# Optimization experiments

Measured on AMD Instinct MI355X. Metric: run time of the kernel, lower is better.

## Reference

```python
import jax, jax.numpy as jnp
import numpy as np

N, E, B = 30000, 240000, 64
F, H, T = 64, 4, 3
BOT = 256


def _gat_layer(x, e_src, e_dst, lin_w, att_src, att_dst, bias):
    # x: [N, in]; lin_w: [in, H*F]; att_*: [H, F]; bias: [H*F]
    xs = (x @ lin_w).reshape(N, H, F)                     # [N,H,F]
    a_src = jnp.einsum('nhf,hf->nh', xs, att_src)         # [N,H]
    a_dst = jnp.einsum('nhf,hf->nh', xs, att_dst)
    logits = jax.nn.leaky_relu(a_src[e_src] + a_dst[e_dst], negative_slope=0.2)  # [E2,H]
    m = jax.ops.segment_max(logits, e_dst, num_segments=N)        # softmax over in-edges per dst
    ex = jnp.exp(logits - m[e_dst])
    denom = jax.ops.segment_sum(ex, e_dst, num_segments=N)
    alpha = ex / (denom[e_dst] + 1e-16)                   # [E2,H]
    msg = alpha[:, :, None] * xs[e_src]                   # [E2,H,F]
    out = jax.ops.segment_sum(msg, e_dst, num_segments=N).reshape(N, H * F)
    return out + bias


def setup_inputs() -> dict:
    key = jax.random.key(0)
    ks = jax.random.split(key, 20)
    s = 0.1
    inp = {
        'street_feature': jax.random.normal(ks[0], (N, 5), jnp.float32),
        'edge_index': jax.random.randint(ks[1], (2, E), 0, N, dtype=jnp.int64),
        'batch': jnp.sort(jax.random.randint(ks[2], (N,), 0, B, dtype=jnp.int64)),
        'bbox_w': jax.random.normal(ks[3], (5, F), jnp.float32) * s,
        'bbox_b': jnp.zeros((F,), jnp.float32),
        'lin_w0': jax.random.normal(ks[4], (F, H * F), jnp.float32) * s,
        'att_src0': jax.random.normal(ks[5], (H, F), jnp.float32) * s,
        'att_dst0': jax.random.normal(ks[6], (H, F), jnp.float32) * s,
        'bias0': jnp.zeros((H * F,), jnp.float32),
        'lin_w1': jax.random.normal(ks[7], (H * F, H * F), jnp.float32) * s,
        'att_src1': jax.random.normal(ks[8], (H, F), jnp.float32) * s,
        'att_dst1': jax.random.normal(ks[9], (H, F), jnp.float32) * s,
        'bias1': jnp.zeros((H * F,), jnp.float32),
        'lin_w2': jax.random.normal(ks[10], (H * F, H * F), jnp.float32) * s,
        'att_src2': jax.random.normal(ks[11], (H, F), jnp.float32) * s,
        'att_dst2': jax.random.normal(ks[12], (H, F), jnp.float32) * s,
        'bias2': jnp.zeros((H * F,), jnp.float32),
        'agg_w': jax.random.normal(ks[13], (F * (1 + H * T), BOT), jnp.float32) * s,
        'agg_b': jnp.zeros((BOT,), jnp.float32),
    }
    return inp


def reference(street_feature, edge_index, batch,
              bbox_w, bbox_b,
              lin_w0, att_src0, att_dst0, bias0,
              lin_w1, att_src1, att_dst1, bias1,
              lin_w2, att_src2, att_dst2, bias2,
              agg_w, agg_b):
    # add self-loops (PyG GATConv default add_self_loops=True)
    loop = jnp.arange(N, dtype=edge_index.dtype)
    e_src = jnp.concatenate([edge_index[0], loop])
    e_dst = jnp.concatenate([edge_index[1], loop])

    x = jax.nn.relu(street_feature @ bbox_w + bbox_b)            # [N,F]
    g = [jax.ops.segment_max(x, batch, num_segments=B)]          # global max pool

    layers = [(lin_w0, att_src0, att_dst0, bias0),
              (lin_w1, att_src1, att_dst1, bias1),
              (lin_w2, att_src2, att_dst2, bias2)]
    for lw, asrc, adst, b in layers:
        x = jax.nn.relu(_gat_layer(x, e_src, e_dst, lw, asrc, adst, b))  # [N,H*F]
        g.append(jax.ops.segment_max(x, batch, num_segments=B))

    g_embed = jnp.concatenate(g, axis=1)                          # [B, F*(1+H*T)]
    return g_embed @ agg_w + agg_b                                # [B, BOT]
```

## Files before the change

kernel.cpp:

```cpp
#include <hip/hip_runtime.h>
#include <hip/hip_bf16.h>

#define N_NODES 30000
#define N_EDGES 240000
#define NB      64
#define FDIM    64
#define NH      4
#define HF      256
#define E2      (N_EDGES + N_NODES)
#define GCOLS   832
#define BOTD    256
#define DEGCAP  64
#define PSPLIT  16
#define FSPLIT  8

typedef __hip_bfloat16 bf16;
typedef __attribute__((ext_vector_type(8))) short short8;
typedef __attribute__((ext_vector_type(4))) float f32x4;
typedef __attribute__((ext_vector_type(4))) unsigned short u16x4;

__device__ __forceinline__ float b2f(bf16 v) { return __bfloat162float(v); }
__device__ __forceinline__ float bits2f(unsigned short u) {
    return __uint_as_float(((unsigned int)u) << 16);
}

#define ENC_B   7500
#define ADJ_B   1055
#define BOFF_B  118
#define WT0 (HF * FDIM)
#define WT1 (WT0 + HF * HF)
#define WT2 (WT1 + HF * HF)
#define WCONV_B 576
#define PRO_B   (ENC_B + ADJ_B + BOFF_B + WCONV_B)

__global__ __launch_bounds__(256) void prologue_kernel(
        const float* __restrict__ sf, const float* __restrict__ bw,
        const float* __restrict__ bb, bf16* __restrict__ xenc,
        const int* __restrict__ esrc, const int* __restrict__ edst,
        int* __restrict__ deg, unsigned short* __restrict__ adj,
        const int* __restrict__ batch, int* __restrict__ boff,
        const float* __restrict__ w0, const float* __restrict__ w1,
        const float* __restrict__ w2, bf16* __restrict__ wT,
        unsigned int* __restrict__ g) {
    __shared__ float s_pool[4][FDIM];
    int b = blockIdx.x, t = threadIdx.x;
    if (b < ENC_B) {
        int i = b * 256 + t;
        int n = i >> 6, f = i & 63, w = t >> 6;
        float acc = bb[f];
#pragma unroll
        for (int k = 0; k < 5; ++k)
            acc += sf[n * 5 + k] * bw[k * FDIM + f];
        bf16 ob = __float2bfloat16(fmaxf(acc, 0.f));
        xenc[i] = ob;
        s_pool[w][f] = b2f(ob);
        __syncthreads();
        int n0b = b * 4;
        int bA = batch[n0b], bB = batch[n0b + 3];
        if (t < FDIM) {
            if (bA == bB) {
                float m = fmaxf(fmaxf(s_pool[0][t], s_pool[1][t]),
                                fmaxf(s_pool[2][t], s_pool[3][t]));
                atomicMax(&g[bA * GCOLS + t], __float_as_uint(m));
            } else {
#pragma unroll
                for (int ww = 0; ww < 4; ++ww)
                    atomicMax(&g[batch[n0b + ww] * GCOLS + t],
                              __float_as_uint(s_pool[ww][t]));
            }
        }
    } else if (b < ENC_B + ADJ_B) {
        int e = (b - ENC_B) * 256 + t;
        if (e >= E2) return;
        int s, d;
        if (e < N_EDGES) { s = esrc[e]; d = edst[e]; }
        else             { s = d = e - N_EDGES; }
        int pos = atomicAdd(&deg[d], 1);
        if (pos < DEGCAP) adj[d * DEGCAP + pos] = (unsigned short)s;
    } else if (b < ENC_B + ADJ_B + BOFF_B) {
        int n = (b - ENC_B - ADJ_B) * 256 + t;
        if (n >= N_NODES) return;
        int b1 = batch[n];
        int b0 = (n == 0) ? -1 : batch[n - 1];
        for (int x = b0 + 1; x <= b1; ++x) boff[x] = n;
        if (n == N_NODES - 1)
            for (int x = b1 + 1; x <= NB; ++x) boff[x] = N_NODES;
    } else {
        int i = (b - ENC_B - ADJ_B - BOFF_B) * 256 + t;
        if (i < WT0) {
            int n = i / FDIM, k = i - n * FDIM;
            wT[i] = __float2bfloat16(w0[k * HF + n]);
        } else if (i < WT1) {
            int j = i - WT0, n = j >> 8, k = j & 255;
            wT[i] = __float2bfloat16(w1[k * HF + n]);
        } else if (i < WT2) {
            int j = i - WT1, n = j >> 8, k = j & 255;
            wT[i] = __float2bfloat16(w2[k * HF + n]);
        }
    }
}

template <int K>
__global__ __launch_bounds__(256) void gemm_mfma_kernel(
        const bf16* __restrict__ xb, const bf16* __restrict__ wT,
        bf16* __restrict__ y, const float* __restrict__ asrc,
        const float* __restrict__ adst, float* __restrict__ a_s,
        float* __restrict__ a_d) {
    constexpr int T = K / 32;
    __shared__ __align__(16) short lds[3 * 10240];
    int t = threadIdx.x, w = t >> 6, l = t & 63;
    int q = l >> 4, m = l & 15;
    int n0 = blockIdx.x * 64;
    const short* xg = (const short*)xb;
    const short* wg = (const short*)wT;
    int sub = l >> 2;
    int k2g = (l & 3) ^ ((l >> 3) & 3);
    int xq  = q ^ ((m >> 1) & 3);
    long rowA = n0 + 16 * w + sub;

    auto stage = [&](int s) {
        int bb = s % 3;
        int k0 = s * 32;
        __builtin_amdgcn_global_load_lds(
            (const __attribute__((address_space(1))) void*)&xg[rowA * K + k0 + k2g * 8],
            (__attribute__((address_space(3))) void*)&lds[bb * 10240 + w * 512],
            16, 0, 0);
#pragma unroll
        for (int u = 0; u < 4; ++u) {
            int rowB = 64 * w + 16 * u + sub;
            __builtin_amdgcn_global_load_lds(
                (const __attribute__((address_space(1))) void*)&wg[(long)rowB * K + k0 + k2g * 8],
                (__attribute__((address_space(3))) void*)&lds[bb * 10240 + 2048 + (w * 4 + u) * 512],
                16, 0, 0);
        }
    };

    f32x4 acc[4][4];
#pragma unroll
    for (int rt = 0; rt < 4; ++rt)
#pragma unroll
        for (int ct = 0; ct < 4; ++ct)
            acc[rt][ct] = (f32x4){0.f, 0.f, 0.f, 0.f};

    stage(0);
    if (T > 1) stage(1);

#pragma unroll
    for (int s = 0; s < T; ++s) {
        if (s < T - 1) asm volatile("s_waitcnt vmcnt(5)" ::: "memory");
        else           asm volatile("s_waitcnt vmcnt(0)" ::: "memory");
        __builtin_amdgcn_s_barrier();
        __builtin_amdgcn_sched_barrier(0);
        if (s + 2 < T) stage(s + 2);
        const short* Ab = &lds[(s % 3) * 10240];
        const short* Bb = Ab + 2048;
        short8 af[4], bfr[4];
#pragma unroll
        for (int rt = 0; rt < 4; ++rt)
            af[rt] = *(const short8*)&Ab[(16 * rt + m) * 32 + xq * 8];
#pragma unroll
        for (int ct = 0; ct < 4; ++ct)
            bfr[ct] = *(const short8*)&Bb[(64 * w + 16 * ct + m) * 32 + xq * 8];
#pragma unroll
        for (int rt = 0; rt < 4; ++rt)
#pragma unroll
            for (int ct = 0; ct < 4; ++ct)
                acc[rt][ct] = __builtin_amdgcn_mfma_f32_16x16x32_bf16(
                    af[rt], bfr[ct], acc[rt][ct], 0, 0, 0);
    }

#pragma unroll
    for (int rt = 0; rt < 4; ++rt)
#pragma unroll
        for (int reg = 0; reg < 4; ++reg) {
            int row = n0 + 16 * rt + 4 * q + reg;
            if (row < N_NODES) {
#pragma unroll
                for (int ct = 0; ct < 4; ++ct)
                    y[(long)row * HF + 64 * w + 16 * ct + m] =
                        __float2bfloat16(acc[rt][ct][reg]);
            }
        }
    float vs[4], vd[4];
#pragma unroll
    for (int ct = 0; ct < 4; ++ct) {
        vs[ct] = asrc[64 * w + 16 * ct + m];
        vd[ct] = adst[64 * w + 16 * ct + m];
    }
#pragma unroll
    for (int rt = 0; rt < 4; ++rt)
#pragma unroll
        for (int reg = 0; reg < 4; ++reg) {
            float ps = 0.f, pd = 0.f;
#pragma unroll
            for (int ct = 0; ct < 4; ++ct) {
                ps += acc[rt][ct][reg] * vs[ct];
                pd += acc[rt][ct][reg] * vd[ct];
            }
#pragma unroll
            for (int mask = 1; mask <= 8; mask <<= 1) {
                ps += __shfl_xor(ps, mask, 64);
                pd += __shfl_xor(pd, mask, 64);
            }
            if (m == 0) {
                int row = n0 + 16 * rt + 4 * q + reg;
                if (row < N_NODES) {
                    a_s[row * NH + w] = ps;
                    a_d[row * NH + w] = pd;
                }
            }
        }
}

#define EXP_S (DEGCAP + 4)
__global__ __launch_bounds__(256) void agg_kernel(
        const unsigned short* __restrict__ adj, const int* __restrict__ deg,
        const bf16* __restrict__ xs, const float* __restrict__ a_s,
        const float* __restrict__ a_d, const float* __restrict__ bias,
        bf16* __restrict__ xout) {
    int w = threadIdx.x >> 6, l = threadIdx.x & 63;
    int n = blockIdx.x * 4 + w;
    __shared__ unsigned short s_src_all[4][DEGCAP];
    __shared__ float s_ex_all[4][NH][EXP_S];
    unsigned short* s_src = s_src_all[w];
    float (*s_ex)[EXP_S] = s_ex_all[w];
    int dn = min(deg[n], DEGCAP);
    int src_l = 0;
    if (l < dn) {
        src_l = adj[n * DEGCAP + l];
        s_src[l] = (unsigned short)src_l;
    }
    f32x4 ad4 = *(const f32x4*)&a_d[n * NH];
    float ex[NH];
    if (l < dn) {
        f32x4 as4 = *(const f32x4*)&a_s[src_l * NH];
#pragma unroll
        for (int h = 0; h < NH; ++h) {
            float a = as4[h] + ad4[h];
            a = (a > 0.f) ? a : 0.2f * a;
            ex[h] = __expf(a);
        }
    } else {
#pragma unroll
        for (int h = 0; h < NH; ++h) ex[h] = 0.f;
    }
#pragma unroll
    for (int h = 0; h < NH; ++h) {
        float s = ex[h];
#pragma unroll
        for (int off = 32; off > 0; off >>= 1) s += __shfl_xor(s, off, 64);
        s_ex[h][l] = ex[h] * (1.f / (s + 1e-16f));
    }
    __builtin_amdgcn_wave_barrier();
    int hh = l >> 4;
    const float* exh = s_ex[hh];
    const unsigned short* xg = (const unsigned short*)xs;
    f32x4 acc = {0.f, 0.f, 0.f, 0.f};
    int k = 0;
    for (; k + 3 < dn; k += 4) {
        int s0 = s_src[k],     s1 = s_src[k + 1];
        int s2 = s_src[k + 2], s3 = s_src[k + 3];
        float a0 = exh[k],     a1 = exh[k + 1];
        float a2 = exh[k + 2], a3 = exh[k + 3];
        u16x4 v0 = *(const u16x4*)&xg[(long)s0 * HF + 4 * l];
        u16x4 v1 = *(const u16x4*)&xg[(long)s1 * HF + 4 * l];
        u16x4 v2 = *(const u16x4*)&xg[(long)s2 * HF + 4 * l];
        u16x4 v3 = *(const u16x4*)&xg[(long)s3 * HF + 4 * l];
#pragma unroll
        for (int j = 0; j < 4; ++j) {
            acc[j] += a0 * bits2f(v0[j]);
            acc[j] += a1 * bits2f(v1[j]);
            acc[j] += a2 * bits2f(v2[j]);
            acc[j] += a3 * bits2f(v3[j]);
        }
    }
    for (; k < dn; ++k) {
        int s0 = s_src[k];
        float a0 = exh[k];
        u16x4 v0 = *(const u16x4*)&xg[(long)s0 * HF + 4 * l];
#pragma unroll
        for (int j = 0; j < 4; ++j) acc[j] += a0 * bits2f(v0[j]);
    }
    f32x4 b4 = *(const f32x4*)&bias[4 * l];
    u16x4 o;
#pragma unroll
    for (int j = 0; j < 4; ++j) {
        bf16 ob = __float2bfloat16(fmaxf(acc[j] + b4[j], 0.f));
        o[j] = *reinterpret_cast<unsigned short*>(&ob);
    }
    *(u16x4*)((unsigned short*)xout + (long)n * HF + 4 * l) = o;
}

__global__ __launch_bounds__(256) void pool256_kernel(const bf16* __restrict__ x,
                                                      const int* __restrict__ boff,
                                                      unsigned int* __restrict__ g, int goff) {
    int b = blockIdx.x / PSPLIT, part = blockIdx.x % PSPLIT;
    int t = threadIdx.x, w = t >> 6, l = t & 63;
    int s = boff[b], e = boff[b + 1];
    int chunk = (e - s + PSPLIT - 1) / PSPLIT;
    int cs = s + part * chunk, ce = min(cs + chunk, e);
    if (cs >= ce) return;
    __shared__ f32x4 sm[256];
    const unsigned short* xg = (const unsigned short*)x;
    f32x4 v = {0.f, 0.f, 0.f, 0.f};
    for (int n = cs + w; n < ce; n += 4) {
        u16x4 u = *(const u16x4*)&xg[(long)n * HF + 4 * l];
#pragma unroll
        for (int j = 0; j < 4; ++j) v[j] = fmaxf(v[j], bits2f(u[j]));
    }
    sm[t] = v;
    __syncthreads();
    const float* smf = (const float*)sm;
    float m = fmaxf(fmaxf(smf[t], smf[256 + t]), fmaxf(smf[512 + t], smf[768 + t]));
    atomicMax(&g[b * GCOLS + goff + t], __float_as_uint(m));
}

__global__ __launch_bounds__(256) void final_kernel(
        const float* __restrict__ g, const float* __restrict__ w,
        const float* __restrict__ b, float* __restrict__ outp) {
    int bb = blockIdx.x & (NB - 1);
    int slice = blockIdx.x >> 6;
    int j = threadIdx.x;
    const int KS = GCOLS / FSPLIT;
    float acc = (slice == 0) ? b[j] : 0.f;
    int k0 = slice * KS;
    for (int k = k0; k < k0 + KS; ++k)
        acc += g[bb * GCOLS + k] * w[k * BOTD + j];
    atomicAdd(&outp[bb * BOTD + j], acc);
}

extern "C" void kernel_launch(void* const* d_in, const int* in_sizes, int n_in,
                              void* d_out, int out_size, void* d_ws, size_t ws_size,
                              hipStream_t stream) {
    const float* sf     = (const float*)d_in[0];
    const int*   eidx   = (const int*)d_in[1];
    const int*   batch  = (const int*)d_in[2];
    const float* bbox_w = (const float*)d_in[3];
    const float* bbox_b = (const float*)d_in[4];
    const float* lin_w[3] = {(const float*)d_in[5],  (const float*)d_in[9],  (const float*)d_in[13]};
    const float* att_s[3] = {(const float*)d_in[6],  (const float*)d_in[10], (const float*)d_in[14]};
    const float* att_d[3] = {(const float*)d_in[7],  (const float*)d_in[11], (const float*)d_in[15]};
    const float* bias[3]  = {(const float*)d_in[8],  (const float*)d_in[12], (const float*)d_in[16]};
    const float* agg_w  = (const float*)d_in[17];
    const float* agg_b  = (const float*)d_in[18];

    const int* esrc = eidx;
    const int* edst = eidx + N_EDGES;

    char* ws = (char*)d_ws;
    bf16* xsb  = (bf16*)ws;  ws += (size_t)N_NODES * HF * 2;
    bf16* xb0  = (bf16*)ws;  ws += (size_t)N_NODES * HF * 2;
    bf16* xb1  = (bf16*)ws;  ws += (size_t)N_NODES * HF * 2;
    bf16* xenc = (bf16*)ws;  ws += (size_t)N_NODES * FDIM * 2;
    float* a_s = (float*)ws; ws += (size_t)N_NODES * NH * 4;
    float* a_d = (float*)ws; ws += (size_t)N_NODES * NH * 4;
    int*   deg = (int*)ws;   ws += (size_t)N_NODES * 4;
    float* g   = (float*)ws; ws += (size_t)NB * GCOLS * 4;
    int*   boff= (int*)ws;   ws += 1024;
    unsigned short* adj = (unsigned short*)ws; ws += (size_t)N_NODES * DEGCAP * 2;
    bf16* wT   = (bf16*)ws;  ws += (size_t)WT2 * 2;

    hipMemsetAsync(deg, 0, (size_t)N_NODES * 4 + (size_t)NB * GCOLS * 4, stream);
    hipMemsetAsync(d_out, 0, (size_t)NB * BOTD * 4, stream);
    prologue_kernel<<<PRO_B, 256, 0, stream>>>(
        sf, bbox_w, bbox_b, xenc, esrc, edst, deg, adj, batch, boff,
        lin_w[0], lin_w[1], lin_w[2], wT, (unsigned int*)g);

    const bf16* wTl[3] = {wT, wT + WT0, wT + WT1};
    const bf16* xin = xenc;
    bf16* xout = xb0;
    for (int l = 0; l < 3; ++l) {
        if (l == 0)
            gemm_mfma_kernel<FDIM><<<(N_NODES + 63) / 64, 256, 0, stream>>>(
                xin, wTl[l], xsb, att_s[l], att_d[l], a_s, a_d);
        else
            gemm_mfma_kernel<HF><<<(N_NODES + 63) / 64, 256, 0, stream>>>(
                xin, wTl[l], xsb, att_s[l], att_d[l], a_s, a_d);
        agg_kernel<<<N_NODES / 4, 256, 0, stream>>>(adj, deg, xsb, a_s, a_d, bias[l], xout);
        pool256_kernel<<<NB * PSPLIT, 256, 0, stream>>>(xout, boff, (unsigned int*)g, FDIM + l * HF);
        xin = xout;
        xout = (xout == xb0) ? xb1 : xb0;
    }
    final_kernel<<<NB * FSPLIT, 256, 0, stream>>>(g, agg_w, agg_b, (float*)d_out);
}
```

Measured before the change: 274.9 us.

## Load GEMM MFMA operands directly from global memory instead of LDS staging

Removes the triple-buffered LDS pipeline (global_load_lds, vmcnt waits, barriers) from the node-feature GEMM and has each lane load its MFMA fragments straight from global memory. This drops the barriers and LDS traffic and frees LDS for more occupancy. In exchange, operand loads are no longer shared across waves, so A fragments are re-read by all four waves through cache and there is no explicit prefetch overlap.

```diff
diff --git a/kernel.cpp b/kernel.cpp
--- a/kernel.cpp
+++ b/kernel.cpp
@@ -107,33 +107,13 @@
         const float* __restrict__ adst, float* __restrict__ a_s,
         float* __restrict__ a_d) {
     constexpr int T = K / 32;
-    __shared__ __align__(16) short lds[3 * 10240];
     int t = threadIdx.x, w = t >> 6, l = t & 63;
     int q = l >> 4, m = l & 15;
     int n0 = blockIdx.x * 64;
     const short* xg = (const short*)xb;
     const short* wg = (const short*)wT;
-    int sub = l >> 2;
-    int k2g = (l & 3) ^ ((l >> 3) & 3);
-    int xq  = q ^ ((m >> 1) & 3);
-    long rowA = n0 + 16 * w + sub;
-
-    auto stage = [&](int s) {
-        int bb = s % 3;
-        int k0 = s * 32;
-        __builtin_amdgcn_global_load_lds(
-            (const __attribute__((address_space(1))) void*)&xg[rowA * K + k0 + k2g * 8],
-            (__attribute__((address_space(3))) void*)&lds[bb * 10240 + w * 512],
-            16, 0, 0);
-#pragma unroll
-        for (int u = 0; u < 4; ++u) {
-            int rowB = 64 * w + 16 * u + sub;
-            __builtin_amdgcn_global_load_lds(
-                (const __attribute__((address_space(1))) void*)&wg[(long)rowB * K + k0 + k2g * 8],
-                (__attribute__((address_space(3))) void*)&lds[bb * 10240 + 2048 + (w * 4 + u) * 512],
-                16, 0, 0);
-        }
-    };
+    const short* aBase = &xg[(long)(n0 + m) * K + q * 8];
+    const short* bBase = &wg[(long)(64 * w + m) * K + q * 8];
 
     f32x4 acc[4][4];
 #pragma unroll
@@ -142,25 +122,15 @@
         for (int ct = 0; ct < 4; ++ct)
             acc[rt][ct] = (f32x4){0.f, 0.f, 0.f, 0.f};
 
-    stage(0);
-    if (T > 1) stage(1);
-
 #pragma unroll
     for (int s = 0; s < T; ++s) {
-        if (s < T - 1) asm volatile("s_waitcnt vmcnt(5)" ::: "memory");
-        else           asm volatile("s_waitcnt vmcnt(0)" ::: "memory");
-        __builtin_amdgcn_s_barrier();
-        __builtin_amdgcn_sched_barrier(0);
-        if (s + 2 < T) stage(s + 2);
-        const short* Ab = &lds[(s % 3) * 10240];
-        const short* Bb = Ab + 2048;
         short8 af[4], bfr[4];
 #pragma unroll
         for (int rt = 0; rt < 4; ++rt)
-            af[rt] = *(const short8*)&Ab[(16 * rt + m) * 32 + xq * 8];
+            af[rt] = *(const short8*)&aBase[(long)rt * 16 * K + s * 32];
 #pragma unroll
         for (int ct = 0; ct < 4; ++ct)
-            bfr[ct] = *(const short8*)&Bb[(64 * w + 16 * ct + m) * 32 + xq * 8];
+            bfr[ct] = *(const short8*)&bBase[(long)ct * 16 * K + s * 32];
 #pragma unroll
         for (int rt = 0; rt < 4; ++rt)
 #pragma unroll
```

Measured after the change: 292.6 us. +6.4%, slower.
